# Optimization experiments

Measured on AMD Instinct MI355X. Metric: run time of the kernel, lower is better.

## Reference

```python
import jax, jax.numpy as jnp
import numpy as np

IN_CH = 1024
OUT_CH = 1024
N_SUBJECTS = 32
B = 512


def setup_inputs() -> dict:
    key = jax.random.key(0)
    k_x, k_w, k_b, k_idx = jax.random.split(key, 4)
    scale = 1.0 / (IN_CH ** 0.5)
    x = jax.random.normal(k_x, (B, IN_CH), dtype=jnp.float32)
    weights = jax.random.normal(k_w, (N_SUBJECTS, IN_CH, OUT_CH), dtype=jnp.float32) * scale
    bias = jax.random.normal(k_b, (N_SUBJECTS, OUT_CH), dtype=jnp.float32) * scale
    subject_idx = jax.random.randint(k_idx, (B,), 0, N_SUBJECTS, dtype=jnp.int64)
    return {"x": x, "subject_idx": subject_idx, "weights": weights, "bias": bias}


def reference(x, subject_idx, weights, bias):
    # gather per-sample weight [B,C,D] and bias [B,D]
    w = weights[subject_idx]          # [B, C, D]
    b = bias[subject_idx]             # [B, D]
    out = jnp.einsum('bc,bcd->bd', x, w) + b
    return out
```

## Files before the change

kernel.cpp:

```cpp
#include <hip/hip_runtime.h>
#include <hip/hip_bf16.h>


typedef float f4v __attribute__((ext_vector_type(4)));

#define N_SUBJ 32
#define B_ROWS 512
#define IN_CH_K 1024
#define OUT_CH_K 1024
#define ROWS_PER_CHUNK 16
#define MAX_CHUNKS 64
#define CSEGS 4
#define CSEG 256
#define WSLICE 64
#define DTILES 4
#define DTILE 256
#define XPAD 20

#define ENT_OFF 1
#define PERM_OFF 256
#define PART_OFF_F 1024
#define PART_FLOATS (CSEGS * B_ROWS * OUT_CH_K)
#define WS_NEED_BYTES (4096 + (size_t)PART_FLOATS * 4)

__global__ __launch_bounds__(512) void build_groups(
    const int* __restrict__ idx, int* __restrict__ ws)
{
    __shared__ int counts[N_SUBJ];
    __shared__ int offs[N_SUBJ];
    __shared__ int cursor[N_SUBJ];
    const int t = threadIdx.x;
    if (t < N_SUBJ) counts[t] = 0;
    __syncthreads();
    const int s = idx[t] & (N_SUBJ - 1);
    atomicAdd(&counts[s], 1);
    __syncthreads();
    if (t == 0) {
        int acc = 0, nch = 0;
        for (int i = 0; i < N_SUBJ; ++i) {
            offs[i] = acc;
            cursor[i] = acc;
            acc += counts[i];
        }
        for (int i = 0; i < N_SUBJ; ++i) {
            for (int st = 0; st < counts[i]; st += ROWS_PER_CHUNK) {
                int c = counts[i] - st;
                if (c > ROWS_PER_CHUNK) c = ROWS_PER_CHUNK;
                ws[ENT_OFF + nch * 3 + 0] = i;
                ws[ENT_OFF + nch * 3 + 1] = offs[i] + st;
                ws[ENT_OFF + nch * 3 + 2] = c;
                ++nch;
            }
        }
        ws[0] = nch;
    }
    __syncthreads();
    const int pos = atomicAdd(&cursor[s], 1);
    ws[PERM_OFF + pos] = t;
}

__global__ __launch_bounds__(256) void init_bias(
    const int* __restrict__ idx, const float* __restrict__ bias,
    float* __restrict__ out)
{
    const int b = blockIdx.x;
    const int s = idx[b];
    const int d = threadIdx.x * 4;
    *(float4*)&out[(size_t)b * OUT_CH_K + d] =
        *(const float4*)&bias[(size_t)s * OUT_CH_K + d];
}

#define GLOAD(dst, ptr) \
    asm volatile("global_load_dwordx4 %0, %1, off" : "=v"(dst) : "v"(ptr))
#define WAIT_VM(n) do { \
    asm volatile("s_waitcnt vmcnt(" #n ")" ::: "memory"); \
    __builtin_amdgcn_sched_barrier(0); } while (0)

#define CSTEP(wreg, cidx) { \
    const float4 x0 = ((const float4*)&xst[cidx][0])[0]; \
    const float4 x1 = ((const float4*)&xst[cidx][0])[1]; \
    const float4 x2 = ((const float4*)&xst[cidx][0])[2]; \
    const float4 x3 = ((const float4*)&xst[cidx][0])[3]; \
    acc[ 0] += wreg * x0.x;  acc[ 1] += wreg * x0.y; \
    acc[ 2] += wreg * x0.z;  acc[ 3] += wreg * x0.w; \
    acc[ 4] += wreg * x1.x;  acc[ 5] += wreg * x1.y; \
    acc[ 6] += wreg * x1.z;  acc[ 7] += wreg * x1.w; \
    acc[ 8] += wreg * x2.x;  acc[ 9] += wreg * x2.y; \
    acc[10] += wreg * x2.z;  acc[11] += wreg * x2.w; \
    acc[12] += wreg * x3.x;  acc[13] += wreg * x3.y; \
    acc[14] += wreg * x3.z;  acc[15] += wreg * x3.w; }

template<bool ATOMIC>
__global__ __launch_bounds__(256, 3) void subject_gemm(
    const float* __restrict__ x, const float* __restrict__ W,
    const int* __restrict__ ws, float* __restrict__ ws_part,
    float* __restrict__ out)
{
    const int chunk = blockIdx.x;
    if (chunk >= ws[0]) return;
    const int s     = ws[ENT_OFF + chunk * 3 + 0];
    const int start = ws[ENT_OFF + chunk * 3 + 1];
    const int cnt   = ws[ENT_OFF + chunk * 3 + 2];
    const int cbase = blockIdx.y * CSEG;
    const int dbase = blockIdx.z * DTILE;

    __shared__ float xst[CSEG][XPAD];
    __shared__ int rowidx[ROWS_PER_CHUNK];

    const int t = threadIdx.x;
    if (t < ROWS_PER_CHUNK)
        rowidx[t] = (t < cnt) ? ws[PERM_OFF + start + t] : -1;
    __syncthreads();

    #pragma unroll
    for (int r = 0; r < ROWS_PER_CHUNK; ++r) {
        const int row = rowidx[r];
        xst[t][r] = (row >= 0) ? x[(size_t)row * IN_CH_K + cbase + t] : 0.0f;
    }
    __syncthreads();

    const int lane = t & 63;
    const int wave = t >> 6;
    const int cs   = wave * WSLICE;
    const int d    = dbase + lane * 4;
    const float* wp = W + (size_t)s * (IN_CH_K * OUT_CH_K)
                        + (size_t)(cbase + cs) * OUT_CH_K + d;

    f4v acc[16];
    #pragma unroll
    for (int r = 0; r < 16; ++r) acc[r] = (f4v){0.f, 0.f, 0.f, 0.f};
    f4v wa0, wa1, wa2, wa3, wb0, wb1, wb2, wb3;

    GLOAD(wa0, wp + 0 * OUT_CH_K);
    GLOAD(wa1, wp + 1 * OUT_CH_K);
    GLOAD(wa2, wp + 2 * OUT_CH_K);
    GLOAD(wa3, wp + 3 * OUT_CH_K);
    GLOAD(wb0, wp + 4 * OUT_CH_K);
    GLOAD(wb1, wp + 5 * OUT_CH_K);
    GLOAD(wb2, wp + 6 * OUT_CH_K);
    GLOAD(wb3, wp + 7 * OUT_CH_K);

    #pragma unroll 1
    for (int cb = 0; cb < WSLICE - 8; cb += 8) {
        WAIT_VM(4);
        CSTEP(wa0, cs + cb + 0)
        CSTEP(wa1, cs + cb + 1)
        CSTEP(wa2, cs + cb + 2)
        CSTEP(wa3, cs + cb + 3)
        const float* wn = wp + (size_t)(cb + 8) * OUT_CH_K;
        GLOAD(wa0, wn + 0 * OUT_CH_K);
        GLOAD(wa1, wn + 1 * OUT_CH_K);
        GLOAD(wa2, wn + 2 * OUT_CH_K);
        GLOAD(wa3, wn + 3 * OUT_CH_K);
        WAIT_VM(4);
        CSTEP(wb0, cs + cb + 4)
        CSTEP(wb1, cs + cb + 5)
        CSTEP(wb2, cs + cb + 6)
        CSTEP(wb3, cs + cb + 7)
        GLOAD(wb0, wn + 4 * OUT_CH_K);
        GLOAD(wb1, wn + 5 * OUT_CH_K);
        GLOAD(wb2, wn + 6 * OUT_CH_K);
        GLOAD(wb3, wn + 7 * OUT_CH_K);
    }
    {
        const int cb = WSLICE - 8;
        WAIT_VM(4);
        CSTEP(wa0, cs + cb + 0)
        CSTEP(wa1, cs + cb + 1)
        CSTEP(wa2, cs + cb + 2)
        CSTEP(wa3, cs + cb + 3)
        WAIT_VM(0);
        CSTEP(wb0, cs + cb + 4)
        CSTEP(wb1, cs + cb + 5)
        CSTEP(wb2, cs + cb + 6)
        CSTEP(wb3, cs + cb + 7)
    }

    __syncthreads();
    float (*obuf)[DTILE] = (float(*)[DTILE])&xst[0][0];
    if (wave == 0) {
        #pragma unroll
        for (int r = 0; r < 16; ++r)
            *(f4v*)&obuf[r][lane * 4] = acc[r];
    }
    __syncthreads();
    #pragma unroll
    for (int w = 1; w < 4; ++w) {
        if (wave == w) {
            #pragma unroll
            for (int r = 0; r < 16; ++r) {
                f4v v = *(const f4v*)&obuf[r][lane * 4];
                *(f4v*)&obuf[r][lane * 4] = v + acc[r];
            }
        }
        __syncthreads();
    }

    #pragma unroll
    for (int i = 0; i < 4; ++i) {
        const int r = wave * 4 + i;
        const int row = rowidx[r];
        if (row >= 0) {
            const f4v v = *(const f4v*)&obuf[r][lane * 4];
            if (ATOMIC) {
                float* o = &out[(size_t)row * OUT_CH_K + d];
                atomicAdd(o + 0, v.x); atomicAdd(o + 1, v.y);
                atomicAdd(o + 2, v.z); atomicAdd(o + 3, v.w);
            } else {
                *(f4v*)&ws_part[((size_t)blockIdx.y * B_ROWS + row)
                                * OUT_CH_K + d] = v;
            }
        }
    }
}

__global__ __launch_bounds__(256) void reduce_parts(
    const int* __restrict__ idx, const float* __restrict__ bias,
    const float* __restrict__ part, float* __restrict__ out)
{
    const int b = blockIdx.x;
    const int s = idx[b];
    const int d = threadIdx.x * 4;
    float4 a = *(const float4*)&bias[(size_t)s * OUT_CH_K + d];
    #pragma unroll
    for (int k = 0; k < CSEGS; ++k) {
        const float4 p = *(const float4*)
            &part[((size_t)k * B_ROWS + b) * OUT_CH_K + d];
        a.x += p.x; a.y += p.y; a.z += p.z; a.w += p.w;
    }
    *(float4*)&out[(size_t)b * OUT_CH_K + d] = a;
}

extern "C" void kernel_launch(void* const* d_in, const int* in_sizes, int n_in,
                              void* d_out, int out_size, void* d_ws, size_t ws_size,
                              hipStream_t stream) {
    const float* x    = (const float*)d_in[0];
    const int*   idx  = (const int*)d_in[1];
    const float* W    = (const float*)d_in[2];
    const float* bias = (const float*)d_in[3];
    float* out = (float*)d_out;
    int* ws = (int*)d_ws;
    float* ws_part = (float*)ws + PART_OFF_F;

    build_groups<<<1, 512, 0, stream>>>(idx, ws);

    dim3 grid(MAX_CHUNKS, CSEGS, DTILES);
    if (ws_size >= WS_NEED_BYTES) {
        subject_gemm<false><<<grid, 256, 0, stream>>>(x, W, ws, ws_part, out);
        reduce_parts<<<B_ROWS, 256, 0, stream>>>(idx, bias, ws_part, out);
    } else {
        init_bias<<<B_ROWS, 256, 0, stream>>>(idx, bias, out);
        subject_gemm<true><<<grid, 256, 0, stream>>>(x, W, ws, ws_part, out);
    }
}
```

Before: 226.3 us.

## Raise rows per chunk to 24 and use atomic output instead of partial reduction

Each subject chunk now holds up to 24 rows instead of 16, so with about 16 rows per subject on average most subjects fit in one chunk and their weight slice is streamed once rather than twice. The workspace partial-sum buffer and the separate reduce kernel are dropped. Bias is pre-initialized and each C-segment block atomically adds into the output. The cost is more accumulator registers (occupancy hint lowered from 3 to 2 blocks), wasted FMAs on padded rows, and float atomics that make summation order nondeterministic.

```diff
diff --git a/kernel.cpp b/kernel.cpp
--- a/kernel.cpp
+++ b/kernel.cpp
@@ -8,20 +8,17 @@
 #define B_ROWS 512
 #define IN_CH_K 1024
 #define OUT_CH_K 1024
-#define ROWS_PER_CHUNK 16
+#define RPC 24
 #define MAX_CHUNKS 64
 #define CSEGS 4
 #define CSEG 256
 #define WSLICE 64
 #define DTILES 4
 #define DTILE 256
-#define XPAD 20
+#define XPAD 28
 
 #define ENT_OFF 1
 #define PERM_OFF 256
-#define PART_OFF_F 1024
-#define PART_FLOATS (CSEGS * B_ROWS * OUT_CH_K)
-#define WS_NEED_BYTES (4096 + (size_t)PART_FLOATS * 4)
 
 __global__ __launch_bounds__(512) void build_groups(
     const int* __restrict__ idx, int* __restrict__ ws)
@@ -43,9 +40,9 @@
             acc += counts[i];
         }
         for (int i = 0; i < N_SUBJ; ++i) {
-            for (int st = 0; st < counts[i]; st += ROWS_PER_CHUNK) {
+            for (int st = 0; st < counts[i]; st += RPC) {
                 int c = counts[i] - st;
-                if (c > ROWS_PER_CHUNK) c = ROWS_PER_CHUNK;
+                if (c > RPC) c = RPC;
                 ws[ENT_OFF + nch * 3 + 0] = i;
                 ws[ENT_OFF + nch * 3 + 1] = offs[i] + st;
                 ws[ENT_OFF + nch * 3 + 2] = c;
@@ -81,6 +78,8 @@
     const float4 x1 = ((const float4*)&xst[cidx][0])[1]; \
     const float4 x2 = ((const float4*)&xst[cidx][0])[2]; \
     const float4 x3 = ((const float4*)&xst[cidx][0])[3]; \
+    const float4 x4 = ((const float4*)&xst[cidx][0])[4]; \
+    const float4 x5 = ((const float4*)&xst[cidx][0])[5]; \
     acc[ 0] += wreg * x0.x;  acc[ 1] += wreg * x0.y; \
     acc[ 2] += wreg * x0.z;  acc[ 3] += wreg * x0.w; \
     acc[ 4] += wreg * x1.x;  acc[ 5] += wreg * x1.y; \
@@ -88,13 +87,15 @@
     acc[ 8] += wreg * x2.x;  acc[ 9] += wreg * x2.y; \
     acc[10] += wreg * x2.z;  acc[11] += wreg * x2.w; \
     acc[12] += wreg * x3.x;  acc[13] += wreg * x3.y; \
-    acc[14] += wreg * x3.z;  acc[15] += wreg * x3.w; }
-
-template<bool ATOMIC>
-__global__ __launch_bounds__(256, 3) void subject_gemm(
+    acc[14] += wreg * x3.z;  acc[15] += wreg * x3.w; \
+    acc[16] += wreg * x4.x;  acc[17] += wreg * x4.y; \
+    acc[18] += wreg * x4.z;  acc[19] += wreg * x4.w; \
+    acc[20] += wreg * x5.x;  acc[21] += wreg * x5.y; \
+    acc[22] += wreg * x5.z;  acc[23] += wreg * x5.w; }
+
+__global__ __launch_bounds__(256, 2) void subject_gemm(
     const float* __restrict__ x, const float* __restrict__ W,
-    const int* __restrict__ ws, float* __restrict__ ws_part,
-    float* __restrict__ out)
+    const int* __restrict__ ws, float* __restrict__ out)
 {
     const int chunk = blockIdx.x;
     if (chunk >= ws[0]) return;
@@ -105,15 +106,15 @@
     const int dbase = blockIdx.z * DTILE;
 
     __shared__ float xst[CSEG][XPAD];
-    __shared__ int rowidx[ROWS_PER_CHUNK];
+    __shared__ int rowidx[RPC];
 
     const int t = threadIdx.x;
-    if (t < ROWS_PER_CHUNK)
+    if (t < RPC)
         rowidx[t] = (t < cnt) ? ws[PERM_OFF + start + t] : -1;
     __syncthreads();
 
     #pragma unroll
-    for (int r = 0; r < ROWS_PER_CHUNK; ++r) {
+    for (int r = 0; r < RPC; ++r) {
         const int row = rowidx[r];
         xst[t][r] = (row >= 0) ? x[(size_t)row * IN_CH_K + cbase + t] : 0.0f;
     }
@@ -126,9 +127,9 @@
     const float* wp = W + (size_t)s * (IN_CH_K * OUT_CH_K)
                         + (size_t)(cbase + cs) * OUT_CH_K + d;
 
-    f4v acc[16];
-    #pragma unroll
-    for (int r = 0; r < 16; ++r) acc[r] = (f4v){0.f, 0.f, 0.f, 0.f};
+    f4v acc[RPC];
+    #pragma unroll
+    for (int r = 0; r < RPC; ++r) acc[r] = (f4v){0.f, 0.f, 0.f, 0.f};
     f4v wa0, wa1, wa2, wa3, wb0, wb1, wb2, wb3;
 
     GLOAD(wa0, wp + 0 * OUT_CH_K);
@@ -180,7 +181,7 @@
     float (*obuf)[DTILE] = (float(*)[DTILE])&xst[0][0];
     if (wave == 0) {
         #pragma unroll
-        for (int r = 0; r < 16; ++r)
+        for (int r = 0; r < RPC; ++r)
             *(f4v*)&obuf[r][lane * 4] = acc[r];
     }
     __syncthreads();
@@ -188,7 +189,7 @@
     for (int w = 1; w < 4; ++w) {
         if (wave == w) {
             #pragma unroll
-            for (int r = 0; r < 16; ++r) {
+            for (int r = 0; r < RPC; ++r) {
                 f4v v = *(const f4v*)&obuf[r][lane * 4];
                 *(f4v*)&obuf[r][lane * 4] = v + acc[r];
             }
@@ -197,38 +198,16 @@
     }
 
     #pragma unroll
-    for (int i = 0; i < 4; ++i) {
-        const int r = wave * 4 + i;
+    for (int i = 0; i < 6; ++i) {
+        const int r = wave * 6 + i;
         const int row = rowidx[r];
         if (row >= 0) {
             const f4v v = *(const f4v*)&obuf[r][lane * 4];
-            if (ATOMIC) {
-                float* o = &out[(size_t)row * OUT_CH_K + d];
-                atomicAdd(o + 0, v.x); atomicAdd(o + 1, v.y);
-                atomicAdd(o + 2, v.z); atomicAdd(o + 3, v.w);
-            } else {
-                *(f4v*)&ws_part[((size_t)blockIdx.y * B_ROWS + row)
-                                * OUT_CH_K + d] = v;
-            }
-        }
-    }
-}
-
-__global__ __launch_bounds__(256) void reduce_parts(
-    const int* __restrict__ idx, const float* __restrict__ bias,
-    const float* __restrict__ part, float* __restrict__ out)
-{
-    const int b = blockIdx.x;
-    const int s = idx[b];
-    const int d = threadIdx.x * 4;
-    float4 a = *(const float4*)&bias[(size_t)s * OUT_CH_K + d];
-    #pragma unroll
-    for (int k = 0; k < CSEGS; ++k) {
-        const float4 p = *(const float4*)
-            &part[((size_t)k * B_ROWS + b) * OUT_CH_K + d];
-        a.x += p.x; a.y += p.y; a.z += p.z; a.w += p.w;
-    }
-    *(float4*)&out[(size_t)b * OUT_CH_K + d] = a;
+            float* o = &out[(size_t)row * OUT_CH_K + d];
+            atomicAdd(o + 0, v.x); atomicAdd(o + 1, v.y);
+            atomicAdd(o + 2, v.z); atomicAdd(o + 3, v.w);
+        }
+    }
 }
 
 extern "C" void kernel_launch(void* const* d_in, const int* in_sizes, int n_in,
@@ -240,16 +219,10 @@
     const float* bias = (const float*)d_in[3];
     float* out = (float*)d_out;
     int* ws = (int*)d_ws;
-    float* ws_part = (float*)ws + PART_OFF_F;
 
     build_groups<<<1, 512, 0, stream>>>(idx, ws);
+    init_bias<<<B_ROWS, 256, 0, stream>>>(idx, bias, out);
 
     dim3 grid(MAX_CHUNKS, CSEGS, DTILES);
-    if (ws_size >= WS_NEED_BYTES) {
-        subject_gemm<false><<<grid, 256, 0, stream>>>(x, W, ws, ws_part, out);
-        reduce_parts<<<B_ROWS, 256, 0, stream>>>(idx, bias, ws_part, out);
-    } else {
-        init_bias<<<B_ROWS, 256, 0, stream>>>(idx, bias, out);
-        subject_gemm<true><<<grid, 256, 0, stream>>>(x, W, ws, ws_part, out);
-    }
-}
+    subject_gemm<<<grid, 256, 0, stream>>>(x, W, ws, out);
+}
```

After: 234.6 us. 3.7% more time.
